# Optimization experiments

Hardware: AMD Instinct MI355X
Metric: run time of the kernel (lower is better)

## Reference

```python
import jax, jax.numpy as jnp
import numpy as np

N = 50000       # nodes
E = 800000      # edges (before self-loops)
G = 512         # graphs in batch
IN_DIM = 128
OUT_DIM = 8
DIMS = [(IN_DIM, 32), (32, 64), (64, 128), (128, 64)]
EPS = 1e-5


def setup_inputs() -> dict:
    key = jax.random.key(0)
    ks = jax.random.split(key, 40)
    def nrm(k, shape, s=0.05):
        return jax.random.normal(k, shape, jnp.float32) * s
    inp = {}
    inp["x"] = jax.random.normal(ks[0], (N, IN_DIM), jnp.float32)
    inp["edge_index"] = jax.random.randint(ks[1], (2, E), 0, N, dtype=jnp.int32)
    inp["batch"] = jnp.sort(jax.random.randint(ks[2], (N,), 0, G, dtype=jnp.int32))
    for i, (din, dout) in enumerate(DIMS, 1):
        inp[f"W{i}"]  = nrm(ks[3 * i + 0], (din, dout))
        inp[f"as{i}"] = nrm(ks[3 * i + 1], (dout,))
        inp[f"ad{i}"] = nrm(ks[3 * i + 2], (dout,))
        inp[f"b{i}"]  = jnp.zeros((dout,), jnp.float32)
        inp[f"g{i}"]  = jnp.ones((dout,), jnp.float32)   # BN gamma
        inp[f"be{i}"] = jnp.zeros((dout,), jnp.float32)  # BN beta
    inp["Wf"] = nrm(ks[20], (64, 32)); inp["bf"] = jnp.zeros((32,), jnp.float32)
    inp["Wc"] = nrm(ks[21], (32, OUT_DIM)); inp["bc"] = jnp.zeros((OUT_DIM,), jnp.float32)
    return inp


def gat_conv(x, src, dst, W, a_s, a_d, b):
    """PyG GATConv, heads=1: linear (no bias) -> per-edge attention with
    leaky_relu(0.2) -> segment softmax over incoming edges -> scatter-add -> bias."""
    h = x @ W                                   # [N, F]
    a_src = h @ a_s                             # [N]
    a_dst = h @ a_d                             # [N]
    e = jax.nn.leaky_relu(a_src[src] + a_dst[dst], 0.2)   # [E+N]
    m = jax.ops.segment_max(e, dst, num_segments=N)
    w = jnp.exp(e - m[dst])
    denom = jax.ops.segment_sum(w, dst, num_segments=N)
    alpha = w / denom[dst]                      # self-loops guarantee denom > 0
    out = jax.ops.segment_sum(alpha[:, None] * h[src], dst, num_segments=N)
    return out + b


def batch_norm(x, g, be):
    mu = x.mean(axis=0)
    var = x.var(axis=0)                         # biased, as torch training BN
    return (x - mu) * jax.lax.rsqrt(var + EPS) * g + be


def reference(x, edge_index, batch,
              W1, as1, ad1, b1, g1, be1,
              W2, as2, ad2, b2, g2, be2,
              W3, as3, ad3, b3, g3, be3,
              W4, as4, ad4, b4, g4, be4,
              Wf, bf, Wc, bc):
    loops = jnp.arange(N, dtype=edge_index.dtype)
    src = jnp.concatenate([edge_index[0], loops])   # GATConv adds self-loops
    dst = jnp.concatenate([edge_index[1], loops])
    params = [(W1, as1, ad1, b1, g1, be1), (W2, as2, ad2, b2, g2, be2),
              (W3, as3, ad3, b3, g3, be3), (W4, as4, ad4, b4, g4, be4)]
    h = x
    for (W, a_s, a_d, b, g, be) in params:
        h = jax.nn.leaky_relu(gat_conv(h, src, dst, W, a_s, a_d, b), 0.01)
        h = batch_norm(h, g, be)
    pooled = jax.ops.segment_sum(h, batch, num_segments=G)   # global_add_pool
    z = jax.nn.leaky_relu(pooled @ Wf + bf, 0.01)
    return jax.nn.sigmoid(z @ Wc + bc)
```

## Files before the change

### kernel.cpp

```cpp
#include <hip/hip_runtime.h>
#include <math.h>

constexpr int BLK = 256;
constexpr int NBLKA = 256;

static inline int cdiv(long a, long b) { return (int)((a + b - 1) / b); }

typedef __attribute__((ext_vector_type(8))) short short8;
typedef __attribute__((ext_vector_type(4))) float floatx4;

__device__ __forceinline__ unsigned short f2bf(float f) {
    unsigned u = __float_as_uint(f);
    unsigned r = u + 0x7fffu + ((u >> 16) & 1u);
    return (unsigned short)(r >> 16);
}
__device__ __forceinline__ float bf2f(unsigned short s) {
    return __uint_as_float(((unsigned)s) << 16);
}


__global__ void histA_k(const int* __restrict__ dst, int* __restrict__ histg,
                        int E, int nbkt, int chunk) {
    __shared__ int h[256];
    int tid = threadIdx.x, z = blockIdx.x;
    h[tid] = 0;
    __syncthreads();
    int e0 = z * chunk, e1 = min(E, e0 + chunk);
    for (int e = e0 + tid; e < e1; e += BLK) atomicAdd(&h[dst[e] >> 8], 1);
    __syncthreads();
    if (tid < nbkt) histg[z * nbkt + tid] = h[tid];
}

__global__ void blk_scan2_k(int* __restrict__ histg, int* __restrict__ bsum, int nbkt) {
    __shared__ int s[BLK];
    int t = threadIdx.x, b = blockIdx.x;
    int v = histg[t * nbkt + b];
    s[t] = v;
    __syncthreads();
    for (int o = 1; o < BLK; o <<= 1) {
        int tv = (t >= o) ? s[t - o] : 0;
        __syncthreads();
        s[t] += tv;
        __syncthreads();
    }
    histg[t * nbkt + b] = s[t] - v;
    if (t == BLK - 1) bsum[b] = s[t];
}

__global__ void scan_base_k(const int* __restrict__ bsum, int* __restrict__ bucket_base,
                            int nbkt, int E, int* __restrict__ gs, int* __restrict__ ge,
                            int G, float* __restrict__ bnstats) {
    __shared__ int s[BLK];
    int t = threadIdx.x;
    int v = (t < nbkt) ? bsum[t] : 0;
    s[t] = v;
    __syncthreads();
    for (int o = 1; o < BLK; o <<= 1) {
        int tv = (t >= o) ? s[t - o] : 0;
        __syncthreads();
        s[t] += tv;
        __syncthreads();
    }
    if (t < nbkt) bucket_base[t] = s[t] - v;
    if (t == 0) bucket_base[nbkt] = E;
    for (int i = t; i < G; i += BLK) { gs[i] = 0x7fffffff; ge[i] = -1; }
    for (int i = t; i < 8192; i += BLK) bnstats[i] = 0.f;
}

__global__ void scatterA_k(const int* __restrict__ src, const int* __restrict__ dst,
                           const int* __restrict__ histg, const int* __restrict__ bucket_base,
                           unsigned* __restrict__ ebkt, int E, int nbkt, int chunk) {
    __shared__ int cur[256];
    int tid = threadIdx.x, z = blockIdx.x;
    if (tid < nbkt) cur[tid] = histg[z * nbkt + tid] + bucket_base[tid];
    __syncthreads();
    int e0 = z * chunk, e1 = min(E, e0 + chunk);
    for (int e = e0 + tid; e < e1; e += BLK) {
        int d = dst[e];
        int b = d >> 8;
        int pos = atomicAdd(&cur[b], 1);
        ebkt[pos] = ((unsigned)(d & 255) << 16) | (unsigned)src[e];
    }
}

__global__ void csrB_k(const unsigned* __restrict__ ebkt, const int* __restrict__ bucket_base,
                       int* __restrict__ off, unsigned short* __restrict__ csr,
                       const int* __restrict__ batch, int* __restrict__ gs,
                       int* __restrict__ ge, int N, int E, int nbkt) {
    __shared__ int dg[256];
    __shared__ int sc[256];
    int t = threadIdx.x, b = blockIdx.x;
    int n0 = b << 8;
    int cnt = min(256, N - n0);
    dg[t] = (t < cnt) ? 1 : 0;
    __syncthreads();
    int e0 = bucket_base[b], e1 = bucket_base[b + 1];
    for (int e = e0 + t; e < e1; e += BLK) atomicAdd(&dg[ebkt[e] >> 16], 1);
    __syncthreads();
    int d = dg[t];
    sc[t] = d;
    __syncthreads();
    for (int o = 1; o < BLK; o <<= 1) {
        int tv = (t >= o) ? sc[t - o] : 0;
        __syncthreads();
        sc[t] += tv;
        __syncthreads();
    }
    int loff = sc[t] - d;
    int csrbase = e0 + n0;
    if (t < cnt) {
        off[n0 + t] = csrbase + loff;
        csr[csrbase + loff] = (unsigned short)(n0 + t);
        dg[t] = loff + 1;
    }
    if (b == nbkt - 1 && t == 0) off[N] = E + N;
    int n = n0 + t;
    if (n < N) {
        int bb = batch[n];
        if (n == 0) gs[bb] = 0;
        else {
            int pb = batch[n - 1];
            if (pb != bb) { gs[bb] = n; ge[pb] = n - 1; }
        }
        if (n == N - 1) ge[bb] = N - 1;
    }
    __syncthreads();
    for (int e = e0 + t; e < e1; e += BLK) {
        unsigned w = ebkt[e];
        int pos = atomicAdd(&dg[w >> 16], 1);
        csr[csrbase + pos] = (unsigned short)(w & 0xffff);
    }
}

template <int K, int NOUT, bool AFP32, bool HASBN>
__launch_bounds__(256)
__global__ void gemm_fused(const void* __restrict__ av, const float* __restrict__ W,
                           const float* __restrict__ a_s, const float* __restrict__ a_d,
                           const float* __restrict__ bnst, const float* __restrict__ g_prev,
                           const float* __restrict__ be_prev, float invN,
                           unsigned short* __restrict__ hb,
                           float* __restrict__ asrc, float* __restrict__ adst, int N) {
    constexpr int KF = K / 32;
    constexpr int NY = NOUT / 16;
    __shared__ float s_sca[K], s_scc[K], s_rs[K], s_rd[K], s_bd[2];
    int tid = threadIdx.x;
    if (tid < K) {
        float a = 1.f, c = 0.f;
        if (HASBN) {
            float su = 0.f, sq = 0.f;
#pragma unroll
            for (int s = 0; s < 8; ++s) {
                su += bnst[s * 256 + tid];
                sq += bnst[s * 256 + 128 + tid];
            }
            float mu = su * invN;
            float var = sq * invN - mu * mu;
            a = g_prev[tid] * rsqrtf(var + 1e-5f);
            c = be_prev[tid] - mu * a;
        }
        s_sca[tid] = a; s_scc[tid] = c;
    }
    __syncthreads();
    {
        if (tid < K) {
            const float* wr = W + (long)tid * NOUT;
            float rs = 0.f, rd = 0.f;
            for (int f = 0; f < NOUT; ++f) {
                float w = wr[f];
                rs += w * a_s[f];
                rd += w * a_d[f];
            }
            s_rs[tid] = rs; s_rd[tid] = rd;
        }
        __syncthreads();
        if (tid < 2) {
            const float* r = tid ? s_rd : s_rs;
            float b = 0.f;
            for (int k = 0; k < K; ++k) b += s_scc[k] * r[k];
            s_bd[tid] = b;
        }
        __syncthreads();
    }

    int wave = tid >> 6;
    int lane = tid & 63;
    int quad = lane >> 4;
    int r16 = lane & 15;
    int blockbase = blockIdx.x * 128;

    short8 afr[2][KF];
    bool valid[2];
#pragma unroll
    for (int rt = 0; rt < 2; ++rt) {
        int tilebase = blockbase + wave * 32 + rt * 16;
        valid[rt] = tilebase < N;
        if (!valid[rt]) continue;
        int arow = min(tilebase + r16, N - 1);
        if (AFP32) {
            const float* xr = (const float*)av + (long)arow * K;
#pragma unroll
            for (int kk = 0; kk < KF; ++kk) {
                float4 x0 = *(const float4*)(xr + kk * 32 + quad * 8);
                float4 x1 = *(const float4*)(xr + kk * 32 + quad * 8 + 4);
                short8 a;
                a[0] = (short)f2bf(x0.x); a[1] = (short)f2bf(x0.y);
                a[2] = (short)f2bf(x0.z); a[3] = (short)f2bf(x0.w);
                a[4] = (short)f2bf(x1.x); a[5] = (short)f2bf(x1.y);
                a[6] = (short)f2bf(x1.z); a[7] = (short)f2bf(x1.w);
                afr[rt][kk] = a;
            }
        } else {
            const unsigned short* hr = (const unsigned short*)av + (long)arow * K;
#pragma unroll
            for (int kk = 0; kk < KF; ++kk)
                afr[rt][kk] = *(const short8*)(hr + kk * 32 + quad * 8);
        }
        float ds = 0.f, dd = 0.f;
#pragma unroll
        for (int kk = 0; kk < KF; ++kk) {
            int kb = kk * 32 + quad * 8;
#pragma unroll
            for (int j = 0; j < 8; ++j) {
                int k = kb + j;
                float a = bf2f((unsigned short)afr[rt][kk][j]) * s_sca[k];
                ds += a * s_rs[k];
                dd += a * s_rd[k];
            }
        }
        ds += __shfl_xor(ds, 16, 64); ds += __shfl_xor(ds, 32, 64);
        dd += __shfl_xor(dd, 16, 64); dd += __shfl_xor(dd, 32, 64);
        int drow = tilebase + r16;
        if (quad == 0 && drow < N) {
            asrc[drow] = ds + s_bd[0];
            adst[drow] = dd + s_bd[1];
        }
    }

#pragma unroll
    for (int y = 0; y < NY; ++y) {
        int col = y * 16 + r16;
        short8 bfr[KF];
        float biasp = 0.f;
#pragma unroll
        for (int kk = 0; kk < KF; ++kk) {
            short8 b;
#pragma unroll
            for (int j = 0; j < 8; ++j) {
                int k = kk * 32 + quad * 8 + j;
                float w = W[(long)k * NOUT + col];
                b[j] = (short)f2bf(s_sca[k] * w);
                biasp += s_scc[k] * w;
            }
            bfr[kk] = b;
        }
        biasp += __shfl_xor(biasp, 16, 64);
        biasp += __shfl_xor(biasp, 32, 64);

#pragma unroll
        for (int rt = 0; rt < 2; ++rt) {
            if (!valid[rt]) continue;
            int tilebase = blockbase + wave * 32 + rt * 16;
            floatx4 acc = {0.f, 0.f, 0.f, 0.f};
#pragma unroll
            for (int kk = 0; kk < KF; ++kk)
                acc = __builtin_amdgcn_mfma_f32_16x16x32_bf16(afr[rt][kk], bfr[kk], acc, 0, 0, 0);
#pragma unroll
            for (int rr = 0; rr < 4; ++rr) {
                int srow = tilebase + quad * 4 + rr;
                if (srow < N) hb[(long)srow * NOUT + col] = f2bf(acc[rr] + biasp);
            }
        }
    }
}

template <int DOUT, int FPL>
__global__ void gather_fused(const int* __restrict__ off,
                             const unsigned short* __restrict__ csr,
                             const float* __restrict__ asrc, const float* __restrict__ adst,
                             const unsigned short* __restrict__ hb,
                             const float* __restrict__ b,
                             unsigned short* __restrict__ out, int N) {
    constexpr int TPN = DOUT / FPL;
    constexpr int NV = FPL / 8;
    int t = blockIdx.x * blockDim.x + threadIdx.x;
    int d = t / TPN;
    if (d >= N) return;
    int l = t % TPN;
    int p0 = off[d], p1 = off[d + 1];
    float ad = adst[d];
    const int f0 = l * FPL;

    float acc[FPL];
#pragma unroll
    for (int i = 0; i < FPL; ++i) acc[i] = 0.f;
    float sum = 0.f;

#pragma unroll 2
    for (int p = p0; p < p1; ++p) {
        int s = csr[p];
        float e = asrc[s] + ad;
        e = e > 0.f ? e : 0.2f * e;
        float w = __expf(e);
        sum += w;
        const unsigned short* hr = hb + (long)s * DOUT + f0;
#pragma unroll
        for (int v = 0; v < NV; ++v) {
            const uint4 hv = *(const uint4*)(hr + v * 8);
            acc[v * 8 + 0] += w * bf2f((unsigned short)(hv.x & 0xffff));
            acc[v * 8 + 1] += w * bf2f((unsigned short)(hv.x >> 16));
            acc[v * 8 + 2] += w * bf2f((unsigned short)(hv.y & 0xffff));
            acc[v * 8 + 3] += w * bf2f((unsigned short)(hv.y >> 16));
            acc[v * 8 + 4] += w * bf2f((unsigned short)(hv.z & 0xffff));
            acc[v * 8 + 5] += w * bf2f((unsigned short)(hv.z >> 16));
            acc[v * 8 + 6] += w * bf2f((unsigned short)(hv.w & 0xffff));
            acc[v * 8 + 7] += w * bf2f((unsigned short)(hv.w >> 16));
        }
    }
    float inv = 1.f / sum;

#pragma unroll
    for (int v = 0; v < NV; ++v) {
        float4 b0 = *(const float4*)(b + f0 + v * 8);
        float4 b1 = *(const float4*)(b + f0 + v * 8 + 4);
        float bbv[8] = {b0.x, b0.y, b0.z, b0.w, b1.x, b1.y, b1.z, b1.w};
        unsigned pk[4];
#pragma unroll
        for (int i = 0; i < 4; ++i) {
            float v0 = acc[v * 8 + 2 * i] * inv + bbv[2 * i];
            float v1 = acc[v * 8 + 2 * i + 1] * inv + bbv[2 * i + 1];
            v0 = v0 > 0.f ? v0 : 0.01f * v0;
            v1 = v1 > 0.f ? v1 : 0.01f * v1;
            pk[i] = (unsigned)f2bf(v0) | ((unsigned)f2bf(v1) << 16);
        }
        *(uint4*)(out + (long)d * DOUT + f0 + v * 8) = uint4{pk[0], pk[1], pk[2], pk[3]};
    }
}

template <int DOUT>
__global__ void stats_k(const unsigned short* __restrict__ y, float* __restrict__ bn, int N) {
    constexpr int QPR = DOUT / 8;
    __shared__ float ssum[DOUT];
    __shared__ float ssq[DOUT];
    for (int i = threadIdx.x; i < DOUT; i += blockDim.x) { ssum[i] = 0.f; ssq[i] = 0.f; }
    __syncthreads();
    long total = (long)N * QPR;
    long stride = (long)gridDim.x * blockDim.x;
    long t0 = (long)blockIdx.x * blockDim.x + threadIdx.x;
    int f0 = (int)(t0 % QPR) * 8;
    float ls[8], lq[8];
#pragma unroll
    for (int i = 0; i < 8; ++i) { ls[i] = 0.f; lq[i] = 0.f; }
    for (long t = t0; t < total; t += stride) {
        uint4 hv = *(const uint4*)(y + t * 8);
        unsigned vv[4] = {hv.x, hv.y, hv.z, hv.w};
#pragma unroll
        for (int q = 0; q < 4; ++q) {
            float v0 = bf2f((unsigned short)(vv[q] & 0xffff));
            float v1 = bf2f((unsigned short)(vv[q] >> 16));
            ls[2 * q] += v0;     lq[2 * q] += v0 * v0;
            ls[2 * q + 1] += v1; lq[2 * q + 1] += v1 * v1;
        }
    }
#pragma unroll
    for (int i = 0; i < 8; ++i) {
        atomicAdd(&ssum[f0 + i], ls[i]);
        atomicAdd(&ssq[f0 + i], lq[i]);
    }
    __syncthreads();
    float* base = bn + (blockIdx.x & 7) * 256;
    for (int i = threadIdx.x; i < DOUT; i += blockDim.x) {
        atomicAdd(&base[i], ssum[i]);
        atomicAdd(&base[128 + i], ssq[i]);
    }
}

__global__ void pool_head_k(const unsigned short* __restrict__ h, const int* __restrict__ gs,
                            const int* __restrict__ ge, const float* __restrict__ bnst,
                            const float* __restrict__ g4, const float* __restrict__ be4,
                            float invN, const float* __restrict__ Wf,
                            const float* __restrict__ bf, const float* __restrict__ Wc,
                            const float* __restrict__ bc, float* __restrict__ out) {
    int g = blockIdx.x;
    int t = threadIdx.x;
    int f = t & 63, sub = t >> 6;
    __shared__ float pp[4][64];
    __shared__ float p[64];
    __shared__ float z[32];
    int s0 = gs[g], s1 = ge[g];
    float acc = 0.f;
    if (s0 <= s1)
        for (int n = s0 + sub; n <= s1; n += 4) acc += bf2f(h[(long)n * 64 + f]);
    pp[sub][f] = acc;
    __syncthreads();
    if (t < 64) {
        float su = 0.f, sq = 0.f;
#pragma unroll
        for (int s = 0; s < 8; ++s) {
            su += bnst[s * 256 + t];
            sq += bnst[s * 256 + 128 + t];
        }
        float mu = su * invN;
        float var = sq * invN - mu * mu;
        float a = g4[t] * rsqrtf(var + 1e-5f);
        float c = be4[t] - mu * a;
        float cnt = (s0 <= s1) ? (float)(s1 - s0 + 1) : 0.f;
        p[t] = a * (pp[0][t] + pp[1][t] + pp[2][t] + pp[3][t]) + cnt * c;
    }
    __syncthreads();
    if (t < 32) {
        float zacc = bf[t];
#pragma unroll
        for (int ff = 0; ff < 64; ++ff) zacc += p[ff] * Wf[ff * 32 + t];
        z[t] = zacc > 0.f ? zacc : 0.01f * zacc;
    }
    __syncthreads();
    if (t < 8) {
        float oacc = bc[t];
#pragma unroll
        for (int o = 0; o < 32; ++o) oacc += z[o] * Wc[o * 8 + t];
        out[(long)g * 8 + t] = 1.f / (1.f + __expf(-oacc));
    }
}

extern "C" void kernel_launch(void* const* d_in, const int* in_sizes, int n_in,
                              void* d_out, int out_size, void* d_ws, size_t ws_size,
                              hipStream_t stream) {
    const float* x   = (const float*)d_in[0];
    const int* ei    = (const int*)d_in[1];
    const int* batch = (const int*)d_in[2];
    const int N  = in_sizes[2];
    const int E  = in_sizes[1] / 2;
    const int ET = E + N;
    const int G  = out_size / 8;
    const int* src = ei;
    const int* dst = ei + E;

    const float *W[4], *as_[4], *ad_[4], *bb[4], *gg[4], *be_[4];
    for (int i = 0; i < 4; ++i) {
        W[i]   = (const float*)d_in[3 + 6 * i];
        as_[i] = (const float*)d_in[4 + 6 * i];
        ad_[i] = (const float*)d_in[5 + 6 * i];
        bb[i]  = (const float*)d_in[6 + 6 * i];
        gg[i]  = (const float*)d_in[7 + 6 * i];
        be_[i] = (const float*)d_in[8 + 6 * i];
    }
    const float* Wf = (const float*)d_in[27];
    const float* bfp = (const float*)d_in[28];
    const float* Wc = (const float*)d_in[29];
    const float* bc = (const float*)d_in[30];

    float* ws = (float*)d_ws;
    long off_ = 0;
    auto alloc = [&](long nelem) { float* p = ws + off_; off_ += (nelem + 3) & ~3L; return p; };
    unsigned short* h2a = (unsigned short*)alloc((long)N * 64);
    unsigned short* h2b = (unsigned short*)alloc((long)N * 64);
    unsigned short* hb  = (unsigned short*)alloc((long)N * 64);
    float* asrc     = alloc(N);
    float* adst     = alloc(N);
    float* bnstats  = alloc(4 * 2048);
    unsigned* ebkt  = (unsigned*)alloc(E);
    int* histg      = (int*)alloc((long)NBLKA * 256);
    int* bucket_base = (int*)alloc(260);
    int* bsum       = (int*)alloc(256);
    int* off        = (int*)alloc(N + 1);
    unsigned short* csr = (unsigned short*)alloc(ET / 2 + 2);
    int* gs         = (int*)alloc(G);
    int* ge         = (int*)alloc(G);
    (void)ws_size; (void)n_in;

    const int nbkt = cdiv(N, 256);
    const int chunk = cdiv(E, NBLKA);
    const float invN = 1.f / (float)N;

    histA_k<<<NBLKA, BLK, 0, stream>>>(dst, histg, E, nbkt, chunk);
    blk_scan2_k<<<nbkt, BLK, 0, stream>>>(histg, bsum, nbkt);
    scan_base_k<<<1, BLK, 0, stream>>>(bsum, bucket_base, nbkt, E, gs, ge, G, bnstats);
    scatterA_k<<<NBLKA, BLK, 0, stream>>>(src, dst, histg, bucket_base, ebkt, E, nbkt, chunk);
    csrB_k<<<nbkt, BLK, 0, stream>>>(ebkt, bucket_base, off, csr, batch, gs, ge, N, E, nbkt);

#define LAYER(i, DIN, DOUT, FPL, AFP32, HASBN, INP, OUTP, BNPREV, GPREV, BEPREV)          \
    do {                                                                                  \
        gemm_fused<DIN, DOUT, AFP32, HASBN>                                               \
            <<<cdiv(N, 128), 256, 0, stream>>>(                                           \
                INP, W[i], as_[i], ad_[i], BNPREV, GPREV, BEPREV, invN,                   \
                hb, asrc, adst, N);                                                       \
        gather_fused<DOUT, FPL><<<cdiv((long)N * (DOUT / FPL), BLK), BLK, 0, stream>>>(   \
            off, csr, asrc, adst, hb, bb[i], OUTP, N);                                    \
        stats_k<DOUT><<<240, BLK, 0, stream>>>(OUTP, bnstats + i * 2048, N);              \
    } while (0)

    LAYER(0, 128, 32, 8,  true,  false, x,   h2b, bnstats,            gg[0], be_[0]);
    LAYER(1, 32,  64, 16, false, true,  h2b, h2a, bnstats + 0 * 2048, gg[0], be_[0]);
    LAYER(2, 64, 128, 16, false, true,  h2a, h2b, bnstats + 1 * 2048, gg[1], be_[1]);
    LAYER(3, 128, 64, 16, false, true,  h2b, h2a, bnstats + 2 * 2048, gg[2], be_[2]);
#undef LAYER

    pool_head_k<<<G, 256, 0, stream>>>(h2a, gs, ge, bnstats + 3 * 2048, gg[3], be_[3],
                                       invN, Wf, bfp, Wc, bc, (float*)d_out);
}
```

Before: 353.2 us.

## Fuse batch-norm statistics accumulation into the GAT gather kernel

Removes the separate stats_k pass that re-read each layer's bf16 output. The gather kernel now reduces per-feature sum and sum-of-squares with wave shuffles, accumulates them in shared memory, and adds them into 16 global shards (previously 8) with atomics. This saves one kernel launch and a full read of the activation per layer. In exchange the gather kernel gains a barrier, shuffle work and far more global atomics, since it runs many more blocks than the old 240-block stats pass. The statistics are taken from the fp32 values before bf16 rounding rather than from the stored bf16 values.

```diff
diff --git a/kernel.cpp b/kernel.cpp
--- a/kernel.cpp
+++ b/kernel.cpp
@@ -3,6 +3,7 @@
 
 constexpr int BLK = 256;
 constexpr int NBLKA = 256;
+constexpr int NSH = 16;
 
 static inline int cdiv(long a, long b) { return (int)((a + b - 1) / b); }
 
@@ -64,7 +65,7 @@
     if (t < nbkt) bucket_base[t] = s[t] - v;
     if (t == 0) bucket_base[nbkt] = E;
     for (int i = t; i < G; i += BLK) { gs[i] = 0x7fffffff; ge[i] = -1; }
-    for (int i = t; i < 8192; i += BLK) bnstats[i] = 0.f;
+    for (int i = t; i < 4 * NSH * 256; i += BLK) bnstats[i] = 0.f;
 }
 
 __global__ void scatterA_k(const int* __restrict__ src, const int* __restrict__ dst,
@@ -149,7 +150,7 @@
         if (HASBN) {
             float su = 0.f, sq = 0.f;
 #pragma unroll
-            for (int s = 0; s < 8; ++s) {
+            for (int s = 0; s < NSH; ++s) {
                 su += bnst[s * 256 + tid];
                 sq += bnst[s * 256 + 128 + tid];
             }
@@ -279,15 +280,24 @@
                              const float* __restrict__ asrc, const float* __restrict__ adst,
                              const unsigned short* __restrict__ hb,
                              const float* __restrict__ b,
-                             unsigned short* __restrict__ out, int N) {
+                             unsigned short* __restrict__ out,
+                             float* __restrict__ bn, int N) {
     constexpr int TPN = DOUT / FPL;
     constexpr int NV = FPL / 8;
-    int t = blockIdx.x * blockDim.x + threadIdx.x;
+    __shared__ float sst[2 * DOUT];
+    int tid = threadIdx.x;
+    if (tid < 2 * DOUT) sst[tid] = 0.f;
+    __syncthreads();
+
+    int t = blockIdx.x * blockDim.x + tid;
     int d = t / TPN;
-    if (d >= N) return;
     int l = t % TPN;
-    int p0 = off[d], p1 = off[d + 1];
-    float ad = adst[d];
+    bool active = d < N;
+    int lane = tid & 63;
+
+    int p0 = 0, p1 = 0;
+    float ad = 0.f;
+    if (active) { p0 = off[d]; p1 = off[d + 1]; ad = adst[d]; }
     const int f0 = l * FPL;
 
     float acc[FPL];
@@ -316,7 +326,7 @@
             acc[v * 8 + 7] += w * bf2f((unsigned short)(hv.w >> 16));
         }
     }
-    float inv = 1.f / sum;
+    float inv = active ? (1.f / sum) : 0.f;
 
 #pragma unroll
     for (int v = 0; v < NV; ++v) {
@@ -330,47 +340,34 @@
             float v1 = acc[v * 8 + 2 * i + 1] * inv + bbv[2 * i + 1];
             v0 = v0 > 0.f ? v0 : 0.01f * v0;
             v1 = v1 > 0.f ? v1 : 0.01f * v1;
+            if (!active) { v0 = 0.f; v1 = 0.f; }
+            acc[v * 8 + 2 * i] = v0;
+            acc[v * 8 + 2 * i + 1] = v1;
             pk[i] = (unsigned)f2bf(v0) | ((unsigned)f2bf(v1) << 16);
         }
-        *(uint4*)(out + (long)d * DOUT + f0 + v * 8) = uint4{pk[0], pk[1], pk[2], pk[3]};
-    }
-}
-
-template <int DOUT>
-__global__ void stats_k(const unsigned short* __restrict__ y, float* __restrict__ bn, int N) {
-    constexpr int QPR = DOUT / 8;
-    __shared__ float ssum[DOUT];
-    __shared__ float ssq[DOUT];
-    for (int i = threadIdx.x; i < DOUT; i += blockDim.x) { ssum[i] = 0.f; ssq[i] = 0.f; }
-    __syncthreads();
-    long total = (long)N * QPR;
-    long stride = (long)gridDim.x * blockDim.x;
-    long t0 = (long)blockIdx.x * blockDim.x + threadIdx.x;
-    int f0 = (int)(t0 % QPR) * 8;
-    float ls[8], lq[8];
-#pragma unroll
-    for (int i = 0; i < 8; ++i) { ls[i] = 0.f; lq[i] = 0.f; }
-    for (long t = t0; t < total; t += stride) {
-        uint4 hv = *(const uint4*)(y + t * 8);
-        unsigned vv[4] = {hv.x, hv.y, hv.z, hv.w};
-#pragma unroll
-        for (int q = 0; q < 4; ++q) {
-            float v0 = bf2f((unsigned short)(vv[q] & 0xffff));
-            float v1 = bf2f((unsigned short)(vv[q] >> 16));
-            ls[2 * q] += v0;     lq[2 * q] += v0 * v0;
-            ls[2 * q + 1] += v1; lq[2 * q + 1] += v1 * v1;
-        }
-    }
-#pragma unroll
-    for (int i = 0; i < 8; ++i) {
-        atomicAdd(&ssum[f0 + i], ls[i]);
-        atomicAdd(&ssq[f0 + i], lq[i]);
-    }
-    __syncthreads();
-    float* base = bn + (blockIdx.x & 7) * 256;
-    for (int i = threadIdx.x; i < DOUT; i += blockDim.x) {
-        atomicAdd(&base[i], ssum[i]);
-        atomicAdd(&base[128 + i], ssq[i]);
+        if (active)
+            *(uint4*)(out + (long)d * DOUT + f0 + v * 8) = uint4{pk[0], pk[1], pk[2], pk[3]};
+    }
+
+#pragma unroll
+    for (int i = 0; i < FPL; ++i) {
+        float s = acc[i];
+        float q = s * s;
+#pragma unroll
+        for (int o = TPN; o < 64; o <<= 1) {
+            s += __shfl_xor(s, o, 64);
+            q += __shfl_xor(q, o, 64);
+        }
+        if (lane < TPN) {
+            atomicAdd(&sst[f0 + i], s);
+            atomicAdd(&sst[DOUT + f0 + i], q);
+        }
+    }
+    __syncthreads();
+    if (tid < 2 * DOUT) {
+        float* base = bn + (blockIdx.x & (NSH - 1)) * 256;
+        int idx = (tid < DOUT) ? tid : (128 + tid - DOUT);
+        atomicAdd(&base[idx], sst[tid]);
     }
 }
 
@@ -395,7 +392,7 @@
     if (t < 64) {
         float su = 0.f, sq = 0.f;
 #pragma unroll
-        for (int s = 0; s < 8; ++s) {
+        for (int s = 0; s < NSH; ++s) {
             su += bnst[s * 256 + t];
             sq += bnst[s * 256 + 128 + t];
         }
@@ -457,7 +454,7 @@
     unsigned short* hb  = (unsigned short*)alloc((long)N * 64);
     float* asrc     = alloc(N);
     float* adst     = alloc(N);
-    float* bnstats  = alloc(4 * 2048);
+    float* bnstats  = alloc((long)4 * NSH * 256);
     unsigned* ebkt  = (unsigned*)alloc(E);
     int* histg      = (int*)alloc((long)NBLKA * 256);
     int* bucket_base = (int*)alloc(260);
@@ -485,16 +482,15 @@
                 INP, W[i], as_[i], ad_[i], BNPREV, GPREV, BEPREV, invN,                   \
                 hb, asrc, adst, N);                                                       \
         gather_fused<DOUT, FPL><<<cdiv((long)N * (DOUT / FPL), BLK), BLK, 0, stream>>>(   \
-            off, csr, asrc, adst, hb, bb[i], OUTP, N);                                    \
-        stats_k<DOUT><<<240, BLK, 0, stream>>>(OUTP, bnstats + i * 2048, N);              \
+            off, csr, asrc, adst, hb, bb[i], OUTP, bnstats + (long)i * NSH * 256, N);     \
     } while (0)
 
-    LAYER(0, 128, 32, 8,  true,  false, x,   h2b, bnstats,            gg[0], be_[0]);
-    LAYER(1, 32,  64, 16, false, true,  h2b, h2a, bnstats + 0 * 2048, gg[0], be_[0]);
-    LAYER(2, 64, 128, 16, false, true,  h2a, h2b, bnstats + 1 * 2048, gg[1], be_[1]);
-    LAYER(3, 128, 64, 16, false, true,  h2b, h2a, bnstats + 2 * 2048, gg[2], be_[2]);
+    LAYER(0, 128, 32, 8,  true,  false, x,   h2b, bnstats,                 gg[0], be_[0]);
+    LAYER(1, 32,  64, 16, false, true,  h2b, h2a, bnstats + 0L * NSH * 256, gg[0], be_[0]);
+    LAYER(2, 64, 128, 16, false, true,  h2a, h2b, bnstats + 1L * NSH * 256, gg[1], be_[1]);
+    LAYER(3, 128, 64, 16, false, true,  h2b, h2a, bnstats + 2L * NSH * 256, gg[2], be_[2]);
 #undef LAYER
 
-    pool_head_k<<<G, 256, 0, stream>>>(h2a, gs, ge, bnstats + 3 * 2048, gg[3], be_[3],
+    pool_head_k<<<G, 256, 0, stream>>>(h2a, gs, ge, bnstats + 3L * NSH * 256, gg[3], be_[3],
                                        invN, Wf, bfp, Wc, bc, (float*)d_out);
 }
```

After: 344.6 us. -2.4%, faster.
